# Performance work log

Measured on AMD Instinct MI355X. Metric: run time of the kernel, lower is better.

Reference implementation:

```python
import jax, jax.numpy as jnp
import numpy as np
from jax import lax

D_MODEL, D_STATE, D_CONV, EXPAND = 1024, 16, 4, 2
D_INNER = D_MODEL * EXPAND
LN_EPS = 1e-5


def _silu(v):
    return v * jax.nn.sigmoid(v)


def setup_inputs() -> dict:
    key = jax.random.key(0)
    ks = jax.random.split(key, 12)
    B, T = 4, 2048
    x = jax.random.normal(ks[0], (B, T, D_MODEL), dtype=jnp.float32)
    W_in = jax.random.normal(ks[1], (2 * D_INNER, D_MODEL), dtype=jnp.float32) * (D_MODEL ** -0.5)
    conv_w = jax.random.normal(ks[2], (D_INNER, 1, D_CONV), dtype=jnp.float32) * (D_CONV ** -0.5)
    conv_b = jax.random.normal(ks[3], (D_INNER,), dtype=jnp.float32) * 0.01
    W_x = jax.random.normal(ks[4], (2 * D_STATE, D_INNER), dtype=jnp.float32) * (D_INNER ** -0.5)
    dt_init_std = D_INNER ** -0.5
    W_dt = jax.random.uniform(ks[5], (D_INNER, D_INNER), minval=-dt_init_std, maxval=dt_init_std, dtype=jnp.float32)
    # bias = inverse softplus of dt sampled log-uniform in [dt_min, dt_max]
    dt = jnp.exp(jax.random.uniform(ks[6], (D_INNER,)) * (np.log(0.1) - np.log(0.001)) + np.log(0.001))
    b_dt = dt + jnp.log(-jnp.expm1(-dt))
    A_log = jnp.log(jnp.arange(1, D_STATE + 1, dtype=jnp.float32) * 0.5)
    D_param = jnp.ones((D_INNER,), dtype=jnp.float32)
    W_out = jax.random.normal(ks[7], (D_MODEL, D_INNER), dtype=jnp.float32) * (D_MODEL ** -0.5)
    ln_g = jnp.ones((D_INNER,), dtype=jnp.float32)
    ln_b = jnp.zeros((D_INNER,), dtype=jnp.float32)
    return {"x": x, "W_in": W_in, "conv_w": conv_w, "conv_b": conv_b, "W_x": W_x,
            "W_dt": W_dt, "b_dt": b_dt, "A_log": A_log, "D_param": D_param,
            "W_out": W_out, "ln_g": ln_g, "ln_b": ln_b}


def _forward(x, W_in, conv_w, conv_b, W_x, W_dt, b_dt, A_log, D_param, W_out, ln_g, ln_b):
    B, T, _ = x.shape
    xz = jnp.einsum('btd,ed->bte', x, W_in)            # (B,T,2*d_inner)
    xp, z = xz[..., :D_INNER], xz[..., D_INNER:]
    # depthwise causal conv1d (left pad d_conv-1, keep first T outputs)
    xc = lax.conv_general_dilated(
        jnp.transpose(xp, (0, 2, 1)), conv_w,
        window_strides=(1,), padding=[(D_CONV - 1, 0)],
        feature_group_count=D_INNER,
        dimension_numbers=('NCH', 'OIH', 'NCH')) + conv_b[None, :, None]
    xc = _silu(jnp.transpose(xc, (0, 2, 1)))           # (B,T,d_inner)
    ssm = jnp.einsum('bti,si->bts', xc, W_x)           # (B,T,2*d_state)
    Bp, Cp = ssm[..., :D_STATE], ssm[..., D_STATE:]
    dt = jax.nn.softplus(jnp.einsum('bti,oi->bto', xc, W_dt) + b_dt)
    A = -jnp.exp(A_log)                                # (d_state,)

    def step(h, inp):
        x_t, b_t, c_t, dt_t = inp                      # (B,d),(B,s),(B,s),(B,d)
        dA = jnp.exp(dt_t[..., None] * A)              # (B,d_inner,d_state)
        h = dA * h + (dt_t[..., None] * b_t[:, None, :]) * x_t[..., None]
        y_t = jnp.einsum('bds,bs->bd', h, c_t)
        return h, y_t

    h0 = jnp.zeros((B, D_INNER, D_STATE), dtype=x.dtype)
    tm = lambda a: jnp.moveaxis(a, 1, 0)               # time-major
    _, ys = lax.scan(step, h0, (tm(xc), tm(Bp), tm(Cp), tm(dt)))
    y = jnp.moveaxis(ys, 0, 1)                         # (B,T,d_inner)

    mu = jnp.mean(y, axis=-1, keepdims=True)
    var = jnp.mean((y - mu) ** 2, axis=-1, keepdims=True)
    y = (y - mu) * lax.rsqrt(var + LN_EPS) * ln_g + ln_b
    y = y + xc * D_param
    y = y * _silu(z)
    return jnp.einsum('bti,di->btd', y, W_out)         # dropout is identity (eval)


def reference(x, W_in, conv_w, conv_b, W_x, W_dt, b_dt, A_log, D_param, W_out, ln_g, ln_b):
    return _forward(x, W_in, conv_w, conv_b, W_x, W_dt, b_dt, A_log, D_param, W_out, ln_g, ln_b)
```

## Files before the change

kernel.cpp:

```cpp
#include <hip/hip_runtime.h>
#include <hip/hip_bf16.h>
#include <math.h>
#include <stdint.h>

#define B_SZ 4
#define T_SZ 2048
#define DM   1024
#define DI   2048
#define DS   16
#define BT   (B_SZ*T_SZ)
#define NC   2176

typedef __attribute__((ext_vector_type(8))) short short8;
typedef __attribute__((ext_vector_type(4))) float f32x4;

__device__ __forceinline__ float siluf(float v) { return v / (1.f + __expf(-v)); }
__device__ __forceinline__ float softplusf(float x) {
    return fmaxf(x, 0.f) + log1pf(__expf(-fabsf(x)));
}
__device__ __forceinline__ unsigned short f2b(float f) {
    __hip_bfloat16 h = __float2bfloat16(f);
    return *reinterpret_cast<unsigned short*>(&h);
}
__device__ __forceinline__ float b2f(unsigned short u) {
    unsigned v = (unsigned)u << 16;
    float f;
    __builtin_memcpy(&f, &v, 4);
    return f;
}
__device__ __forceinline__ void gld_lds16(const void* g, void* l) {
    __builtin_amdgcn_global_load_lds(
        (const __attribute__((address_space(1))) unsigned int*)g,
        (__attribute__((address_space(3))) unsigned int*)l,
        16, 0, 0);
}

__global__ __launch_bounds__(256)
void cvt_bf16(const float* __restrict__ src, unsigned short* __restrict__ dst, int n4)
{
    int i = blockIdx.x * 256 + threadIdx.x;
    if (i >= n4) return;
    float4 v = ((const float4*)src)[i];
    ushort4 o;
    o.x = f2b(v.x); o.y = f2b(v.y); o.z = f2b(v.z); o.w = f2b(v.w);
    ((ushort4*)dst)[i] = o;
}

__global__ __launch_bounds__(256)
void cvt_wc(const float* __restrict__ Wdt, const float* __restrict__ Wx,
            unsigned short* __restrict__ dst)
{
    const int n4 = NC * (DI / 4);
    int i = blockIdx.x * 256 + threadIdx.x;
    if (i >= n4) return;
    int row = i >> 9;
    int c4  = i & 511;
    float4 v;
    if (row < 2048)      v = ((const float4*)Wdt)[(size_t)row * 512 + c4];
    else if (row < 2080) v = ((const float4*)Wx)[(size_t)(row - 2048) * 512 + c4];
    else                 v = make_float4(0.f, 0.f, 0.f, 0.f);
    ushort4 o;
    o.x = f2b(v.x); o.y = f2b(v.y); o.z = f2b(v.z); o.w = f2b(v.w);
    ((ushort4*)dst)[i] = o;
}

__global__ __launch_bounds__(512)
void gemm_mfma(const unsigned short* __restrict__ A,
               const unsigned short* __restrict__ Bm,
               int M, int N, int K, int mode,
               const float* __restrict__ bias,
               void* __restrict__ o0, void* __restrict__ o1, void* __restrict__ o2)
{
    __shared__ unsigned short As[2][128 * 32];
    __shared__ unsigned short Bs[2][128 * 32];

    const int npn = N >> 7;
    const int pid = blockIdx.x;
    const int gsz = 16 * npn;
    const int gid = pid / gsz;
    const int pm  = gid * 16 + (pid % 16);
    const int pn  = (pid % gsz) / 16;
    const int bm  = pm * 128;
    const int bn  = pn * 128;

    const int tid  = threadIdx.x;
    const int lane = tid & 63;
    const int wave = tid >> 6;
    const int wm   = (wave >> 2) * 64;
    const int wn   = (wave & 3) * 32;

    f32x4 zero4 = {0.f, 0.f, 0.f, 0.f};
    f32x4 acc[4][2];
#pragma unroll
    for (int i = 0; i < 4; i++)
#pragma unroll
        for (int j = 0; j < 2; j++) acc[i][j] = zero4;

    const int sr = tid >> 2;
    const int sc = (tid & 3) * 8;
    const unsigned short* Ag = A  + (size_t)(bm + sr) * K + sc;
    const unsigned short* Bg = Bm + (size_t)(bn + sr) * K + sc;

    const int fr = lane & 15;
    const int fk = (lane >> 4) * 8;

    gld_lds16(Ag, &As[0][tid * 8]);
    gld_lds16(Bg, &Bs[0][tid * 8]);
    __syncthreads();

    int cur = 0;
    for (int k0 = 0; k0 < K; k0 += 32) {
        if (k0 + 32 < K) {
            gld_lds16(Ag + k0 + 32, &As[cur ^ 1][tid * 8]);
            gld_lds16(Bg + k0 + 32, &Bs[cur ^ 1][tid * 8]);
        }
        short8 af[4], bf[2];
#pragma unroll
        for (int i = 0; i < 4; i++)
            af[i] = *(const short8*)&As[cur][(wm + i * 16 + fr) * 32 + fk];
#pragma unroll
        for (int j = 0; j < 2; j++)
            bf[j] = *(const short8*)&Bs[cur][(wn + j * 16 + fr) * 32 + fk];
#pragma unroll
        for (int i = 0; i < 4; i++)
#pragma unroll
            for (int j = 0; j < 2; j++)
                acc[i][j] = __builtin_amdgcn_mfma_f32_16x16x32_bf16(
                    af[i], bf[j], acc[i][j], 0, 0, 0);
        __syncthreads();
        cur ^= 1;
    }

    const int cr0 = bm + wm + (lane >> 4) * 4;
    const int cc0 = bn + wn + (lane & 15);
#pragma unroll
    for (int i = 0; i < 4; i++) {
#pragma unroll
        for (int j = 0; j < 2; j++) {
            const int col = cc0 + j * 16;
#pragma unroll
            for (int r = 0; r < 4; r++) {
                const int row = cr0 + i * 16 + r;
                float v = acc[i][j][r];
                if (mode == 0) {
                    if (col < 2048)
                        ((unsigned short*)o0)[(size_t)row * 2048 + col] = f2b(v);
                    else
                        ((unsigned short*)o1)[(size_t)row * 2048 + col - 2048] = f2b(v);
                } else if (mode == 1) {
                    if (col < 2048) {
                        ((float*)o0)[(size_t)row * 2048 + col] = softplusf(v + bias[col]);
                    } else if (col < 2064) {
                        ((float*)o1)[(size_t)row * DS + (col - 2048)] = v;
                    } else if (col < 2080) {
                        ((float*)o2)[(size_t)row * DS + (col - 2064)] = v;
                    }
                } else {
                    ((float*)o0)[(size_t)row * N + col] = v;
                }
            }
        }
    }
}

__global__ __launch_bounds__(256)
void conv_silu(const unsigned short* __restrict__ xpb, const float* __restrict__ cw,
               const float* __restrict__ cb, unsigned short* __restrict__ xcb)
{
    const int idx = blockIdx.x * 256 + threadIdx.x;
    const int i  = idx & (DI - 1);
    const int bt = idx >> 11;
    const int t  = bt & (T_SZ - 1);
    float acc = cb[i];
    float4 w = *(const float4*)(cw + (size_t)i * 4);
    float wr[4] = {w.x, w.y, w.z, w.w};
#pragma unroll
    for (int k = 0; k < 4; k++) {
        const int tt = t - 3 + k;
        if (tt >= 0)
            acc = fmaf(b2f(xpb[(size_t)(bt - 3 + k) * DI + i]), wr[k], acc);
    }
    xcb[idx] = f2b(siluf(acc));
}

#define CH 16
#define CL (T_SZ / CH)

__global__ __launch_bounds__(256)
void scan2(const unsigned short* __restrict__ xcb, float* __restrict__ dty,
           const float* __restrict__ Bp, const float* __restrict__ Cp,
           const float* __restrict__ A_log)
{
    __shared__ float shH[CH][16][DS];
    __shared__ float shP[CH][16][DS];
    __shared__ float shI[CH][16][DS];
    const int tid = threadIdx.x;
    const int c = tid >> 4;
    const int g = tid & 15;
    const int b = blockIdx.y;
    const int d = blockIdx.x * 16 + g;

    float A[DS];
#pragma unroll
    for (int s = 0; s < DS; s++) A[s] = -__expf(A_log[s]);

    const size_t colbase = (size_t)b * T_SZ * DI + d;
    const unsigned short* xp = xcb + colbase + (size_t)c * CL * DI;
    float* dp = dty + colbase + (size_t)c * CL * DI;
    const float4* Bb = (const float4*)(Bp + ((size_t)b * T_SZ + c * CL) * DS);
    const float4* Cb = (const float4*)(Cp + ((size_t)b * T_SZ + c * CL) * DS);

    float h[DS], P[DS];
#pragma unroll
    for (int s = 0; s < DS; s++) { h[s] = 0.f; P[s] = 1.f; }

    for (int i = 0; i < CL; i++) {
        const float xv = b2f(xp[(size_t)i * DI]);
        const float dv = dp[(size_t)i * DI];
        float4 Bv[4] = {Bb[i*4+0], Bb[i*4+1], Bb[i*4+2], Bb[i*4+3]};
        const float* bs = (const float*)&Bv[0];
        const float dx = dv * xv;
#pragma unroll
        for (int s = 0; s < DS; s++) {
            const float dA = __expf(dv * A[s]);
            h[s] = fmaf(dA, h[s], dx * bs[s]);
            P[s] *= dA;
        }
    }
#pragma unroll
    for (int s = 0; s < DS; s += 4) {
        *(float4*)&shH[c][g][s] = make_float4(h[s], h[s+1], h[s+2], h[s+3]);
        *(float4*)&shP[c][g][s] = make_float4(P[s], P[s+1], P[s+2], P[s+3]);
    }
    __syncthreads();

    {
        const int g2 = tid >> 4, s2 = tid & 15;
        float hin = 0.f;
        shI[0][g2][s2] = 0.f;
        for (int cc = 1; cc < CH; cc++) {
            hin = fmaf(shP[cc-1][g2][s2], hin, shH[cc-1][g2][s2]);
            shI[cc][g2][s2] = hin;
        }
    }
    __syncthreads();

#pragma unroll
    for (int s = 0; s < DS; s++) h[s] = shI[c][g][s];
    for (int i = 0; i < CL; i++) {
        const float xv = b2f(xp[(size_t)i * DI]);
        const float dv = dp[(size_t)i * DI];
        float4 Bv[4] = {Bb[i*4+0], Bb[i*4+1], Bb[i*4+2], Bb[i*4+3]};
        float4 Cv[4] = {Cb[i*4+0], Cb[i*4+1], Cb[i*4+2], Cb[i*4+3]};
        const float* bs = (const float*)&Bv[0];
        const float* cs = (const float*)&Cv[0];
        const float dx = dv * xv;
        float yv = 0.f;
#pragma unroll
        for (int s = 0; s < DS; s++) {
            const float dA = __expf(dv * A[s]);
            h[s] = fmaf(dA, h[s], dx * bs[s]);
            yv = fmaf(h[s], cs[s], yv);
        }
        dp[(size_t)i * DI] = yv;
    }
}

__global__ __launch_bounds__(256)
void ln_fuse(const float* __restrict__ y, const unsigned short* __restrict__ xcb,
             const unsigned short* __restrict__ zb, const float* __restrict__ g,
             const float* __restrict__ bln, const float* __restrict__ Dp,
             unsigned short* __restrict__ yb)
{
    __shared__ float rs[256], rss[256];
    const int bt  = blockIdx.x;
    const int tid = threadIdx.x;
    const float* yr = y + (size_t)bt * DI;
    const unsigned short* xr = xcb + (size_t)bt * DI;
    const unsigned short* zr = zb + (size_t)bt * DI;
    unsigned short* orow = yb + (size_t)bt * DI;

    float v[8];
    float s = 0.f, ss = 0.f;
#pragma unroll
    for (int j = 0; j < 8; j++) {
        v[j] = yr[tid + j * 256];
        s  += v[j];
        ss += v[j] * v[j];
    }
    rs[tid] = s; rss[tid] = ss;
    __syncthreads();
    for (int off = 128; off > 0; off >>= 1) {
        if (tid < off) { rs[tid] += rs[tid + off]; rss[tid] += rss[tid + off]; }
        __syncthreads();
    }
    const float mu   = rs[0] * (1.f / DI);
    const float var  = rss[0] * (1.f / DI) - mu * mu;
    const float rstd = rsqrtf(var + 1e-5f);
#pragma unroll
    for (int j = 0; j < 8; j++) {
        const int dcol = tid + j * 256;
        float yn = (v[j] - mu) * rstd * g[dcol] + bln[dcol];
        yn += b2f(xr[dcol]) * Dp[dcol];
        yn *= siluf(b2f(zr[dcol]));
        orow[dcol] = f2b(yn);
    }
}

extern "C" void kernel_launch(void* const* d_in, const int* in_sizes, int n_in,
                              void* d_out, int out_size, void* d_ws, size_t ws_size,
                              hipStream_t stream)
{
    const float* x      = (const float*)d_in[0];
    const float* W_in   = (const float*)d_in[1];
    const float* conv_w = (const float*)d_in[2];
    const float* conv_b = (const float*)d_in[3];
    const float* W_x    = (const float*)d_in[4];
    const float* W_dt   = (const float*)d_in[5];
    const float* b_dt   = (const float*)d_in[6];
    const float* A_log  = (const float*)d_in[7];
    const float* D_par  = (const float*)d_in[8];
    const float* W_out  = (const float*)d_in[9];
    const float* ln_g   = (const float*)d_in[10];
    const float* ln_b   = (const float*)d_in[11];
    float* out = (float*)d_out;

    char* w = (char*)d_ws;
    const size_t MB = 1ull << 20;
    unsigned short* xpb    = (unsigned short*)(w);
    unsigned short* zb     = (unsigned short*)(w + 32 * MB);
    unsigned short* xcb    = (unsigned short*)(w + 64 * MB);
    float*          dts    = (float*)(w + 96 * MB);
    unsigned short* xb     = (unsigned short*)(w + 96 * MB);
    unsigned short* W_inb  = (unsigned short*)(w + 112 * MB);
    unsigned short* Wcb    = (unsigned short*)(w + 160 * MB);
    unsigned short* W_outb = (unsigned short*)(w + 169 * MB);
    float*          BpF    = (float*)(w + 174 * MB);
    float*          CpF    = BpF + (size_t)BT * DS;
    unsigned short* yb     = xpb;

    dim3 blk(256);
    dim3 blk512(512);

    cvt_bf16<<<dim3((BT * DM / 4 + 255) / 256), blk, 0, stream>>>(x, xb, BT * DM / 4);
    cvt_bf16<<<dim3((2 * DI * DM / 4 + 255) / 256), blk, 0, stream>>>(W_in, W_inb, 2 * DI * DM / 4);
    cvt_wc<<<dim3((NC * DI / 4 + 255) / 256), blk, 0, stream>>>(W_dt, W_x, Wcb);
    cvt_bf16<<<dim3((DM * DI / 4 + 255) / 256), blk, 0, stream>>>(W_out, W_outb, DM * DI / 4);

    gemm_mfma<<<dim3((BT / 128) * (2 * DI / 128)), blk512, 0, stream>>>(
        xb, W_inb, BT, 2 * DI, DM, 0, nullptr, xpb, zb, nullptr);

    conv_silu<<<dim3(BT * DI / 256), blk, 0, stream>>>(xpb, conv_w, conv_b, xcb);

    gemm_mfma<<<dim3((BT / 128) * (NC / 128)), blk512, 0, stream>>>(
        xcb, Wcb, BT, NC, DI, 1, b_dt, dts, BpF, CpF);

    scan2<<<dim3(DI / 16, B_SZ), blk, 0, stream>>>(xcb, dts, BpF, CpF, A_log);

    ln_fuse<<<dim3(BT), blk, 0, stream>>>(dts, xcb, zb, ln_g, ln_b, D_par, yb);

    gemm_mfma<<<dim3((BT / 128) * (DM / 128)), blk512, 0, stream>>>(
        yb, W_outb, BT, DM, DI, 2, nullptr, out, nullptr, nullptr);
}
```

Baseline: 633.5 us.

## Enlarge GEMM tiles to 256x256 with 4-stage LDS pipeline and swizzled layout

The MFMA GEMM moves from 128x128 to 256x256 block tiles, so each wave now computes a 128x64 sub-tile. LDS staging goes from double to quad buffering, with explicit vmcnt waits, and an XOR swizzle is applied to the LDS layout to avoid bank conflicts. The aim is more data reuse per load and better overlap of global loads with MFMA work. In exchange the kernel uses many more registers (128 accumulator floats per lane) and 128KB of LDS, and there are fewer blocks per GEMM. NC is padded to 2304 so the fused dt/B/C GEMM divides evenly into 256-wide tiles, which adds some padded work.

```diff
diff --git a/kernel.cpp b/kernel.cpp
--- a/kernel.cpp
+++ b/kernel.cpp
@@ -9,7 +9,7 @@
 #define DI   2048
 #define DS   16
 #define BT   (B_SZ*T_SZ)
-#define NC   2176
+#define NC   2304
 
 typedef __attribute__((ext_vector_type(8))) short short8;
 typedef __attribute__((ext_vector_type(4))) float f32x4;
@@ -64,84 +64,118 @@
     ((ushort4*)dst)[i] = o;
 }
 
-__global__ __launch_bounds__(512)
+__global__ __launch_bounds__(512, 2)
 void gemm_mfma(const unsigned short* __restrict__ A,
                const unsigned short* __restrict__ Bm,
                int M, int N, int K, int mode,
                const float* __restrict__ bias,
                void* __restrict__ o0, void* __restrict__ o1, void* __restrict__ o2)
 {
-    __shared__ unsigned short As[2][128 * 32];
-    __shared__ unsigned short Bs[2][128 * 32];
-
-    const int npn = N >> 7;
+    __shared__ unsigned short As[4][256 * 32];
+    __shared__ unsigned short Bs[4][256 * 32];
+
+    const int npn = N >> 8;
     const int pid = blockIdx.x;
-    const int gsz = 16 * npn;
+    const int gsz = 8 * npn;
     const int gid = pid / gsz;
-    const int pm  = gid * 16 + (pid % 16);
-    const int pn  = (pid % gsz) / 16;
-    const int bm  = pm * 128;
-    const int bn  = pn * 128;
+    const int pm  = gid * 8 + (pid % 8);
+    const int pn  = (pid % gsz) / 8;
+    const int bm  = pm * 256;
+    const int bn  = pn * 256;
 
     const int tid  = threadIdx.x;
     const int lane = tid & 63;
     const int wave = tid >> 6;
-    const int wm   = (wave >> 2) * 64;
-    const int wn   = (wave & 3) * 32;
+    const int wm   = (wave >> 2) * 128;
+    const int wn   = (wave & 3) * 64;
+
+    const int srow  = tid >> 2;
+    const int sgran = (tid & 3) ^ ((tid >> 3) & 3);
+    const unsigned short* Ag = A  + (size_t)(bm + srow) * K + sgran * 8;
+    const unsigned short* Bg = Bm + (size_t)(bn + srow) * K + sgran * 8;
+    const size_t rowK = (size_t)128 * K;
+
+    const int fr = lane & 15;
+    const int fg = lane >> 4;
+    int aoff[8], boff[4];
+#pragma unroll
+    for (int m = 0; m < 8; m++) {
+        const int l = (wm + m * 16 + fr) * 64 + fg * 16;
+        aoff[m] = l ^ (((l >> 7) & 3) << 4);
+    }
+#pragma unroll
+    for (int n = 0; n < 4; n++) {
+        const int l = (wn + n * 16 + fr) * 64 + fg * 16;
+        boff[n] = l ^ (((l >> 7) & 3) << 4);
+    }
 
     f32x4 zero4 = {0.f, 0.f, 0.f, 0.f};
-    f32x4 acc[4][2];
-#pragma unroll
-    for (int i = 0; i < 4; i++)
-#pragma unroll
-        for (int j = 0; j < 2; j++) acc[i][j] = zero4;
-
-    const int sr = tid >> 2;
-    const int sc = (tid & 3) * 8;
-    const unsigned short* Ag = A  + (size_t)(bm + sr) * K + sc;
-    const unsigned short* Bg = Bm + (size_t)(bn + sr) * K + sc;
-
-    const int fr = lane & 15;
-    const int fk = (lane >> 4) * 8;
-
-    gld_lds16(Ag, &As[0][tid * 8]);
-    gld_lds16(Bg, &Bs[0][tid * 8]);
-    __syncthreads();
-
-    int cur = 0;
-    for (int k0 = 0; k0 < K; k0 += 32) {
-        if (k0 + 32 < K) {
-            gld_lds16(Ag + k0 + 32, &As[cur ^ 1][tid * 8]);
-            gld_lds16(Bg + k0 + 32, &Bs[cur ^ 1][tid * 8]);
-        }
-        short8 af[4], bf[2];
-#pragma unroll
-        for (int i = 0; i < 4; i++)
-            af[i] = *(const short8*)&As[cur][(wm + i * 16 + fr) * 32 + fk];
-#pragma unroll
-        for (int j = 0; j < 2; j++)
-            bf[j] = *(const short8*)&Bs[cur][(wn + j * 16 + fr) * 32 + fk];
-#pragma unroll
-        for (int i = 0; i < 4; i++)
-#pragma unroll
-            for (int j = 0; j < 2; j++)
-                acc[i][j] = __builtin_amdgcn_mfma_f32_16x16x32_bf16(
-                    af[i], bf[j], acc[i][j], 0, 0, 0);
-        __syncthreads();
-        cur ^= 1;
-    }
-
-    const int cr0 = bm + wm + (lane >> 4) * 4;
-    const int cc0 = bn + wn + (lane & 15);
-#pragma unroll
-    for (int i = 0; i < 4; i++) {
-#pragma unroll
-        for (int j = 0; j < 2; j++) {
-            const int col = cc0 + j * 16;
+    f32x4 acc[8][4];
+#pragma unroll
+    for (int m = 0; m < 8; m++)
+#pragma unroll
+        for (int n = 0; n < 4; n++) acc[m][n] = zero4;
+
+    const int NT = K >> 5;
+
+#define STAGE(b, t) do {                                    \
+        const size_t k0_ = (size_t)(t) * 32;                \
+        gld_lds16(Ag + k0_,        &As[(b)][tid * 8]);      \
+        gld_lds16(Ag + rowK + k0_, &As[(b)][4096 + tid * 8]);\
+        gld_lds16(Bg + k0_,        &Bs[(b)][tid * 8]);      \
+        gld_lds16(Bg + rowK + k0_, &Bs[(b)][4096 + tid * 8]);\
+    } while (0)
+
+    STAGE(0, 0);
+    STAGE(1, 1);
+    STAGE(2, 2);
+
+    for (int t = 0; t < NT; ++t) {
+        if (t + 3 < NT) STAGE((t + 3) & 3, t + 3);
+        const int rem = NT - 1 - t;
+        if (rem >= 3)      asm volatile("s_waitcnt vmcnt(12)" ::: "memory");
+        else if (rem == 2) asm volatile("s_waitcnt vmcnt(8)"  ::: "memory");
+        else if (rem == 1) asm volatile("s_waitcnt vmcnt(4)"  ::: "memory");
+        else               asm volatile("s_waitcnt vmcnt(0)"  ::: "memory");
+        __builtin_amdgcn_s_barrier();
+        asm volatile("" ::: "memory");
+
+        const char* Ab = (const char*)&As[t & 3][0];
+        const char* Bb = (const char*)&Bs[t & 3][0];
+        short8 af[8], bf[4];
+#pragma unroll
+        for (int m = 0; m < 8; m++)
+            af[m] = *(const short8*)(Ab + aoff[m]);
+#pragma unroll
+        for (int n = 0; n < 4; n++)
+            bf[n] = *(const short8*)(Bb + boff[n]);
+
+        __builtin_amdgcn_s_setprio(1);
+#pragma unroll
+        for (int m = 0; m < 8; m++)
+#pragma unroll
+            for (int n = 0; n < 4; n++)
+                acc[m][n] = __builtin_amdgcn_mfma_f32_16x16x32_bf16(
+                    af[m], bf[n], acc[m][n], 0, 0, 0);
+        __builtin_amdgcn_s_setprio(0);
+
+        asm volatile("" ::: "memory");
+        __builtin_amdgcn_s_barrier();
+        asm volatile("" ::: "memory");
+    }
+#undef STAGE
+
+    const int cr0 = bm + wm + fg * 4;
+    const int cc0 = bn + wn + fr;
+#pragma unroll
+    for (int m = 0; m < 8; m++) {
+#pragma unroll
+        for (int n = 0; n < 4; n++) {
+            const int col = cc0 + n * 16;
 #pragma unroll
             for (int r = 0; r < 4; r++) {
-                const int row = cr0 + i * 16 + r;
-                float v = acc[i][j][r];
+                const int row = cr0 + m * 16 + r;
+                float v = acc[m][n][r];
                 if (mode == 0) {
                     if (col < 2048)
                         ((unsigned short*)o0)[(size_t)row * 2048 + col] = f2b(v);
@@ -347,18 +381,18 @@
     cvt_wc<<<dim3((NC * DI / 4 + 255) / 256), blk, 0, stream>>>(W_dt, W_x, Wcb);
     cvt_bf16<<<dim3((DM * DI / 4 + 255) / 256), blk, 0, stream>>>(W_out, W_outb, DM * DI / 4);
 
-    gemm_mfma<<<dim3((BT / 128) * (2 * DI / 128)), blk512, 0, stream>>>(
+    gemm_mfma<<<dim3((BT / 256) * (2 * DI / 256)), blk512, 0, stream>>>(
         xb, W_inb, BT, 2 * DI, DM, 0, nullptr, xpb, zb, nullptr);
 
     conv_silu<<<dim3(BT * DI / 256), blk, 0, stream>>>(xpb, conv_w, conv_b, xcb);
 
-    gemm_mfma<<<dim3((BT / 128) * (NC / 128)), blk512, 0, stream>>>(
+    gemm_mfma<<<dim3((BT / 256) * (NC / 256)), blk512, 0, stream>>>(
         xcb, Wcb, BT, NC, DI, 1, b_dt, dts, BpF, CpF);
 
     scan2<<<dim3(DI / 16, B_SZ), blk, 0, stream>>>(xcb, dts, BpF, CpF, A_log);
 
     ln_fuse<<<dim3(BT), blk, 0, stream>>>(dts, xcb, zb, ln_g, ln_b, D_par, yb);
 
-    gemm_mfma<<<dim3((BT / 128) * (DM / 128)), blk512, 0, stream>>>(
+    gemm_mfma<<<dim3((BT / 256) * (DM / 256)), blk512, 0, stream>>>(
         yb, W_outb, BT, DM, DI, 2, nullptr, out, nullptr, nullptr);
 }
```

Result: slower. 912.0 us (+43.9%).
